# Kernel tuning notes

Measured on AMD Instinct MI355X. Metric: run time of the kernel, lower is better.

Reference implementation:

```python
import jax, jax.numpy as jnp
import numpy as np

B, C, NZ, NY, NX = 4, 64, 1, 496, 432
N_PER = 16000  # pillars per sample


def setup_inputs() -> dict:
    key = jax.random.key(0)
    rng = np.random.default_rng(0)
    coords_list = []
    for b in range(B):
        # unique (y, x) cells per sample so scatter writes never collide
        flat = rng.choice(NY * NX, size=N_PER, replace=False).astype(np.int64)
        y, x = flat // NX, flat % NX
        z = np.zeros(N_PER, np.int64)  # nz == 1 -> z coordinate is always 0
        bb = np.full(N_PER, b, np.int64)
        coords_list.append(np.stack([bb, z, y, x], axis=1))
    coords = jnp.asarray(np.concatenate(coords_list, axis=0))  # [N, 4]
    voxel_features = jax.random.normal(key, (B * N_PER, C), dtype=jnp.float32)
    return {
        "voxel_features": voxel_features,
        "coords": coords,
        "batch_size": B,
        "nz": NZ,
        "ny": NY,
        "nx": NX,
    }


def reference(voxel_features, coords, batch_size, nz, ny, nx):
    # Faithful to torch: per-sample index = y*nz + z*nx + x into a canvas of
    # length nz*ny*nx (note the original's unusual index formula; with nz=1,
    # z=0 this is y*nx + x). We fuse all batches into one scatter using a
    # batch-aware flat index.
    spatial = nz * ny * nx
    c = voxel_features.shape[1]
    flat_idx = (coords[:, 0] * spatial
                + coords[:, 1] * nz
                + coords[:, 2] * nx
                + coords[:, 3])  # [N]
    canvas = jnp.zeros((batch_size * spatial, c), dtype=voxel_features.dtype)
    canvas = canvas.at[flat_idx].set(voxel_features)  # single fused scatter
    # [B, spatial, C] -> [B, C, spatial] -> [B, C*nz, ny, nx]
    canvas = canvas.reshape(batch_size, spatial, c).transpose(0, 2, 1)
    return canvas.reshape(batch_size, c * nz, ny, nx)
```

## Files before the change

kernel.cpp:

```cpp
#include <hip/hip_runtime.h>


__global__ void pps_build_idx(const int* __restrict__ coords,
                              const int* __restrict__ nz_p,
                              const int* __restrict__ ny_p,
                              const int* __restrict__ nx_p,
                              int* __restrict__ idxmap, int n_points) {
    int n = blockIdx.x * blockDim.x + threadIdx.x;
    if (n >= n_points) return;
    int nz = nz_p[0], ny = ny_p[0], nx = nx_p[0];
    long long spatial = (long long)nz * ny * nx;
    int b = coords[4 * n + 0];
    int z = coords[4 * n + 1];
    int y = coords[4 * n + 2];
    int x = coords[4 * n + 3];
    long long cell = b * spatial + (long long)z * nz + (long long)y * nx + x;
    idxmap[cell] = n;
}

__global__ __launch_bounds__(256)
void pps_gather_v2(const float* __restrict__ vf,
                   const int* __restrict__ idxmap,
                   const int* __restrict__ nz_p,
                   const int* __restrict__ ny_p,
                   const int* __restrict__ nx_p,
                   float* __restrict__ out,
                   int C, long long ncells, int c_chunk) {
    const long long spatial = (long long)nz_p[0] * ny_p[0] * nx_p[0];
    const long long nquads = (ncells + 3) >> 2;
    const int c0 = blockIdx.y * c_chunk;
    int cn = C - c0;
    if (cn > c_chunk) cn = c_chunk;
    if (cn <= 0) return;

    for (long long q = blockIdx.x * (long long)blockDim.x + threadIdx.x;
         q < nquads; q += (long long)gridDim.x * blockDim.x) {
        long long cell = q << 2;
        long long b = cell / spatial;
        long long s = cell - b * spatial;

        if (cell + 3 < ncells && s + 3 < spatial) {
            int4 iv = *reinterpret_cast<const int4*>(idxmap + cell);
            const float* px = vf + (long long)(iv.x >= 0 ? iv.x : 0) * C + c0;
            const float* py = vf + (long long)(iv.y >= 0 ? iv.y : 0) * C + c0;
            const float* pz = vf + (long long)(iv.z >= 0 ? iv.z : 0) * C + c0;
            const float* pw = vf + (long long)(iv.w >= 0 ? iv.w : 0) * C + c0;
            float* op = out + (b * C + c0) * spatial + s;
            #pragma unroll 4
            for (int c = 0; c < cn; ++c) {
                float4 o;
                o.x = (iv.x >= 0) ? px[c] : 0.0f;
                o.y = (iv.y >= 0) ? py[c] : 0.0f;
                o.z = (iv.z >= 0) ? pz[c] : 0.0f;
                o.w = (iv.w >= 0) ? pw[c] : 0.0f;
                *reinterpret_cast<float4*>(op) = o;
                op += spatial;
            }
        } else {
            for (int j = 0; j < 4; ++j) {
                long long cc = cell + j;
                if (cc >= ncells) break;
                long long bb = cc / spatial;
                long long ss = cc - bb * spatial;
                int idx = idxmap[cc];
                for (int c = 0; c < cn; ++c)
                    out[(bb * C + c0 + c) * spatial + ss] =
                        (idx >= 0) ? vf[(long long)idx * C + c0 + c] : 0.0f;
            }
        }
    }
}

__global__ void pps_scatter_kernel(const float* __restrict__ vf,
                                   const int* __restrict__ coords,
                                   const int* __restrict__ nz_p,
                                   const int* __restrict__ ny_p,
                                   const int* __restrict__ nx_p,
                                   float* __restrict__ out,
                                   int n_points, int C) {
    int idx = blockIdx.x * blockDim.x + threadIdx.x;
    int total = n_points * C;
    if (idx >= total) return;
    int n = idx / C;
    int c = idx - n * C;
    int nz = nz_p[0], ny = ny_p[0], nx = nx_p[0];
    long long spatial = (long long)nz * ny * nx;
    int b = coords[4 * n + 0];
    int z = coords[4 * n + 1];
    int y = coords[4 * n + 2];
    int x = coords[4 * n + 3];
    long long s = (long long)z * nz + (long long)y * nx + (long long)x;
    out[((long long)b * C + c) * spatial + s] = vf[idx];
}

extern "C" void kernel_launch(void* const* d_in, const int* in_sizes, int n_in,
                              void* d_out, int out_size, void* d_ws, size_t ws_size,
                              hipStream_t stream) {
    const float* vf     = (const float*)d_in[0];
    const int*   coords = (const int*)d_in[1];
    const int*   nz_p   = (const int*)d_in[3];
    const int*   ny_p   = (const int*)d_in[4];
    const int*   nx_p   = (const int*)d_in[5];
    float* out = (float*)d_out;

    int n_points = in_sizes[1] / 4;
    int C        = in_sizes[0] / n_points;
    long long ncells = (long long)out_size / C;
    size_t idx_bytes = (size_t)ncells * sizeof(int);

    if (ws_size >= idx_bytes) {
        int* idxmap = (int*)d_ws;
        hipMemsetAsync(idxmap, 0xFF, idx_bytes, stream);
        {
            int block = 256;
            int grid = (n_points + block - 1) / block;
            pps_build_idx<<<grid, block, 0, stream>>>(coords, nz_p, ny_p, nx_p,
                                                      idxmap, n_points);
        }
        {
            int block = 256;
            int c_chunk = 16;
            if (c_chunk > C) c_chunk = C;
            long long nquads = (ncells + 3) / 4;
            long long gx = (nquads + block - 1) / block;
            if (gx > 0x7FFFFFFF) gx = 0x7FFFFFFF;
            int gy = (C + c_chunk - 1) / c_chunk;
            dim3 grid((unsigned)gx, (unsigned)gy, 1);
            pps_gather_v2<<<grid, block, 0, stream>>>(vf, idxmap, nz_p, ny_p,
                                                      nx_p, out, C, ncells,
                                                      c_chunk);
        }
    } else {
        hipMemsetAsync(d_out, 0, (size_t)out_size * sizeof(float), stream);
        int total = n_points * C;
        int block = 256;
        int grid  = (total + block - 1) / block;
        pps_scatter_kernel<<<grid, block, 0, stream>>>(vf, coords, nz_p, ny_p,
                                                       nx_p, out, n_points, C);
    }
}
```

Before: 52.60 us.

## Gather all channels per thread with float4 reads and register transpose

Removes the channel-chunked 2D grid so that each thread handles four cells across all channels. It reads feature rows as float4 and transposes 4x4 in registers before writing float4 outputs. This cuts repeated idxmap reads and scalar feature loads, and reduces block size to 128. There are fewer total threads with more serial work each, and the grid-stride loop is removed, so a clamped grid would no longer cover every cell.

```diff
diff --git a/kernel.cpp b/kernel.cpp
--- a/kernel.cpp
+++ b/kernel.cpp
@@ -18,55 +18,59 @@
     idxmap[cell] = n;
 }
 
-__global__ __launch_bounds__(256)
-void pps_gather_v2(const float* __restrict__ vf,
+__global__ __launch_bounds__(128)
+void pps_gather_v3(const float* __restrict__ vf,
                    const int* __restrict__ idxmap,
                    const int* __restrict__ nz_p,
                    const int* __restrict__ ny_p,
                    const int* __restrict__ nx_p,
                    float* __restrict__ out,
-                   int C, long long ncells, int c_chunk) {
+                   int C, long long ncells) {
     const long long spatial = (long long)nz_p[0] * ny_p[0] * nx_p[0];
     const long long nquads = (ncells + 3) >> 2;
-    const int c0 = blockIdx.y * c_chunk;
-    int cn = C - c0;
-    if (cn > c_chunk) cn = c_chunk;
-    if (cn <= 0) return;
+    long long q = blockIdx.x * (long long)blockDim.x + threadIdx.x;
+    if (q >= nquads) return;
 
-    for (long long q = blockIdx.x * (long long)blockDim.x + threadIdx.x;
-         q < nquads; q += (long long)gridDim.x * blockDim.x) {
-        long long cell = q << 2;
-        long long b = cell / spatial;
-        long long s = cell - b * spatial;
+    long long cell = q << 2;
+    long long b = cell / spatial;
+    long long s = cell - b * spatial;
 
-        if (cell + 3 < ncells && s + 3 < spatial) {
-            int4 iv = *reinterpret_cast<const int4*>(idxmap + cell);
-            const float* px = vf + (long long)(iv.x >= 0 ? iv.x : 0) * C + c0;
-            const float* py = vf + (long long)(iv.y >= 0 ? iv.y : 0) * C + c0;
-            const float* pz = vf + (long long)(iv.z >= 0 ? iv.z : 0) * C + c0;
-            const float* pw = vf + (long long)(iv.w >= 0 ? iv.w : 0) * C + c0;
-            float* op = out + (b * C + c0) * spatial + s;
-            #pragma unroll 4
-            for (int c = 0; c < cn; ++c) {
-                float4 o;
-                o.x = (iv.x >= 0) ? px[c] : 0.0f;
-                o.y = (iv.y >= 0) ? py[c] : 0.0f;
-                o.z = (iv.z >= 0) ? pz[c] : 0.0f;
-                o.w = (iv.w >= 0) ? pw[c] : 0.0f;
-                *reinterpret_cast<float4*>(op) = o;
-                op += spatial;
-            }
-        } else {
-            for (int j = 0; j < 4; ++j) {
-                long long cc = cell + j;
-                if (cc >= ncells) break;
-                long long bb = cc / spatial;
-                long long ss = cc - bb * spatial;
-                int idx = idxmap[cc];
-                for (int c = 0; c < cn; ++c)
-                    out[(bb * C + c0 + c) * spatial + ss] =
-                        (idx >= 0) ? vf[(long long)idx * C + c0 + c] : 0.0f;
-            }
+    if (cell + 3 < ncells && s + 3 < spatial && (C & 3) == 0) {
+        int4 iv = *reinterpret_cast<const int4*>(idxmap + cell);
+        const bool vx = iv.x >= 0, vy = iv.y >= 0, vz = iv.z >= 0, vw = iv.w >= 0;
+        const float* px = vf + (long long)iv.x * C;
+        const float* py = vf + (long long)iv.y * C;
+        const float* pz = vf + (long long)iv.z * C;
+        const float* pw = vf + (long long)iv.w * C;
+        float* op0 = out + b * (long long)C * spatial + s;
+
+        #pragma unroll 4
+        for (int cc = 0; cc < C; cc += 4) {
+            float4 rx = make_float4(0.f, 0.f, 0.f, 0.f);
+            float4 ry = rx, rz = rx, rw = rx;
+            if (vx) rx = *reinterpret_cast<const float4*>(px + cc);
+            if (vy) ry = *reinterpret_cast<const float4*>(py + cc);
+            if (vz) rz = *reinterpret_cast<const float4*>(pz + cc);
+            if (vw) rw = *reinterpret_cast<const float4*>(pw + cc);
+            float* op = op0 + (long long)cc * spatial;
+            *reinterpret_cast<float4*>(op) = make_float4(rx.x, ry.x, rz.x, rw.x);
+            op += spatial;
+            *reinterpret_cast<float4*>(op) = make_float4(rx.y, ry.y, rz.y, rw.y);
+            op += spatial;
+            *reinterpret_cast<float4*>(op) = make_float4(rx.z, ry.z, rz.z, rw.z);
+            op += spatial;
+            *reinterpret_cast<float4*>(op) = make_float4(rx.w, ry.w, rz.w, rw.w);
+        }
+    } else {
+        for (int j = 0; j < 4; ++j) {
+            long long cc = cell + j;
+            if (cc >= ncells) break;
+            long long bb = cc / spatial;
+            long long ss = cc - bb * spatial;
+            int idx = idxmap[cc];
+            for (int c = 0; c < C; ++c)
+                out[(bb * C + c) * spatial + ss] =
+                    (idx >= 0) ? vf[(long long)idx * C + c] : 0.0f;
         }
     }
 }
@@ -118,17 +122,12 @@
                                                       idxmap, n_points);
         }
         {
-            int block = 256;
-            int c_chunk = 16;
-            if (c_chunk > C) c_chunk = C;
+            int block = 128;
             long long nquads = (ncells + 3) / 4;
             long long gx = (nquads + block - 1) / block;
             if (gx > 0x7FFFFFFF) gx = 0x7FFFFFFF;
-            int gy = (C + c_chunk - 1) / c_chunk;
-            dim3 grid((unsigned)gx, (unsigned)gy, 1);
-            pps_gather_v2<<<grid, block, 0, stream>>>(vf, idxmap, nz_p, ny_p,
-                                                      nx_p, out, C, ncells,
-                                                      c_chunk);
+            pps_gather_v3<<<(int)gx, block, 0, stream>>>(vf, idxmap, nz_p, ny_p,
+                                                         nx_p, out, C, ncells);
         }
     } else {
         hipMemsetAsync(d_out, 0, (size_t)out_size * sizeof(float), stream);
```

New measurement: 47.96 us. 1.1x faster.
